# Kernel tuning notes

Measured on AMD Instinct MI355X. Metric: run time of the kernel, lower is better.

The kernel has to match this reference:

```python
import jax, jax.numpy as jnp
import numpy as np

NUM_ROT = 8
OUT_CH = 128
IN_CH = 128
KSIZE = 3


def _resample(filt, angle):
    """Rotate a (O, I, k, k) filter bank by `angle` via bilinear resampling,
    matching F.affine_grid/F.grid_sample with align_corners=True, zero padding."""
    k = filt.shape[-1]
    c, s = jnp.cos(angle), jnp.sin(angle)
    lin = jnp.linspace(-1.0, 1.0, k)
    gy, gx = jnp.meshgrid(lin, lin, indexing='ij')  # (k, k) output coords
    # theta = [[c, -s, 0], [s, c, 0]] applied to (x, y, 1)
    xs = c * gx - s * gy
    ys = s * gx + c * gy
    ix = (xs + 1.0) * 0.5 * (k - 1)  # normalized -> pixel coords
    iy = (ys + 1.0) * 0.5 * (k - 1)
    x0f, y0f = jnp.floor(ix), jnp.floor(iy)
    x0, y0 = x0f.astype(jnp.int32), y0f.astype(jnp.int32)
    wx, wy = ix - x0f, iy - y0f

    def tap(yi, xi, w):
        valid = ((yi >= 0) & (yi < k) & (xi >= 0) & (xi < k)).astype(filt.dtype)
        yc = jnp.clip(yi, 0, k - 1)
        xc = jnp.clip(xi, 0, k - 1)
        return filt[:, :, yc, xc] * (valid * w)  # (O, I, k, k)

    return (tap(y0, x0, (1 - wy) * (1 - wx)) + tap(y0, x0 + 1, (1 - wy) * wx)
            + tap(y0 + 1, x0, wy * (1 - wx)) + tap(y0 + 1, x0 + 1, wy * wx))


def setup_inputs() -> dict:
    key = jax.random.key(0)
    k1, k2, k3 = jax.random.split(key, 3)
    x = jax.random.normal(k1, (16, IN_CH, 128, 128), jnp.float32)
    # base_conv.weight: (out_channels * num_rotations, in_channels, k, k)
    weight = jax.random.normal(k2, (OUT_CH * NUM_ROT, IN_CH, KSIZE, KSIZE), jnp.float32) * 0.05
    rot_alpha = jax.random.normal(k3, (NUM_ROT,), jnp.float32) * 0.1 + 1.0
    return {"x": x, "weight": weight, "rot_alpha": rot_alpha}


def reference(x, weight, rot_alpha):
    R, O, K = NUM_ROT, OUT_CH, KSIZE
    # weight.view(O, R, I, K, K)[:, i] per rotation -> (R, O, I, K, K)
    w_r = weight.reshape(O, R, -1, K, K).transpose(1, 0, 2, 3, 4)
    angles = rot_alpha * (jnp.pi / 4) * jnp.arange(R, dtype=jnp.float32)
    rot_w = jax.vmap(_resample)(w_r, angles)  # (R, O, I, K, K)
    filters = rot_w.reshape(R * O, -1, K, K)
    # one conv with all rotated filter banks instead of R separate convs
    y = jax.lax.conv_general_dilated(
        x, filters, window_strides=(1, 1),
        padding=[(K // 2, K // 2), (K // 2, K // 2)],
        dimension_numbers=('NCHW', 'OIHW', 'NCHW'))  # (B, R*O, H, W)
    B, _, H, W = y.shape
    return y.reshape(B, R, O, H, W).max(axis=1)  # max over rotations
```

## Files before the change

kernel.cpp:

```cpp
#include <hip/hip_runtime.h>

typedef short short8 __attribute__((ext_vector_type(8)));
typedef float f32x4 __attribute__((ext_vector_type(4)));

#define XP_BYTES (16ull * 130 * 130 * 128 * 2)

static __device__ __forceinline__ unsigned short f2bf(float f) {
  unsigned u = __float_as_uint(f);
  u += 0x7FFFu + ((u >> 16) & 1u);
  return (unsigned short)(u >> 16);
}

static __device__ __forceinline__ void gload16(const void* g, void* l) {
  __builtin_amdgcn_global_load_lds(
      (const __attribute__((address_space(1))) void*)g,
      (__attribute__((address_space(3))) void*)l, 16, 0, 0);
}

static __device__ __forceinline__ float wtap(const float* f, int yi, int xi) {
  bool valid = (yi >= 0) & (yi < 3) & (xi >= 0) & (xi < 3);
  int yc = min(max(yi, 0), 2), xc = min(max(xi, 0), 2);
  return valid ? f[yc * 3 + xc] : 0.f;
}

__global__ __launch_bounds__(256) void wprep_kernel(
    const float* __restrict__ w, const float* __restrict__ rot_alpha,
    unsigned short* __restrict__ w2) {
  int gid = blockIdx.x * 256 + threadIdx.x;
  int ic = gid & 127;
  int nr = gid >> 7;
  int r = nr & 7;
  const float* wf = w + (size_t)nr * (128 * 9) + (size_t)ic * 9;
  float f[9];
#pragma unroll
  for (int q = 0; q < 9; ++q) f[q] = wf[q];
  float ang = rot_alpha[r] * 0.78539816339744830962f * (float)r;
  float sth, cth;
  sincosf(ang, &sth, &cth);
#pragma unroll
  for (int j = 0; j < 3; ++j) {
#pragma unroll
    for (int i = 0; i < 3; ++i) {
      float gy = (float)(j - 1), gx = (float)(i - 1);
      float xs = cth * gx - sth * gy;
      float ys = sth * gx + cth * gy;
      float ix = xs + 1.0f, iy = ys + 1.0f;
      float x0f = floorf(ix), y0f = floorf(iy);
      int x0 = (int)x0f, y0 = (int)y0f;
      float wx = ix - x0f, wy = iy - y0f;
      float acc = wtap(f, y0, x0) * (1.f - wy) * (1.f - wx)
                + wtap(f, y0, x0 + 1) * (1.f - wy) * wx
                + wtap(f, y0 + 1, x0) * wy * (1.f - wx)
                + wtap(f, y0 + 1, x0 + 1) * wy * wx;
      w2[(size_t)nr * 1152 + (size_t)(j * 3 + i) * 128 + ic] = f2bf(acc);
    }
  }
}

__global__ __launch_bounds__(256) void xprep_kernel(
    const float* __restrict__ x, unsigned short* __restrict__ xp) {
  const int yy = blockIdx.x;
  const int b = blockIdx.y;
  const int t = threadIdx.x;
  const size_t rowbase = ((size_t)b * 130 + yy) * (130 * 128);
  if (yy == 0 || yy == 129) {
    uint4 z = {0u, 0u, 0u, 0u};
    for (int i = t; i < 2080; i += 256)
      ((uint4*)(xp + rowbase))[i] = z;
    return;
  }
  const int y = yy - 1;
  __shared__ float lt[32][129];
  if (t < 32) {
    uint4 z = {0u, 0u, 0u, 0u};
    int xx = (t < 16) ? 0 : 129;
    int cc = (t & 15) * 8;
    *(uint4*)(xp + rowbase + (size_t)xx * 128 + cc) = z;
  }
  for (int c0 = 0; c0 < 128; c0 += 32) {
#pragma unroll
    for (int i = 0; i < 16; ++i) {
      int idx = i * 256 + t;
      int c = idx >> 7, wq = idx & 127;
      lt[c][wq] = x[(((size_t)b * 128 + c0 + c) * 128 + y) * 128 + wq];
    }
    __syncthreads();
#pragma unroll
    for (int i = 0; i < 2; ++i) {
      int u = i * 256 + t;
      int xx = u >> 2, cp = (u & 3) * 8;
      unsigned short v[8];
#pragma unroll
      for (int q = 0; q < 8; ++q) v[q] = f2bf(lt[cp + q][xx]);
      *(uint4*)(xp + rowbase + (size_t)(xx + 1) * 128 + c0 + cp) = *(uint4*)v;
    }
    __syncthreads();
  }
}

__global__ __launch_bounds__(512, 2) void conv_kernel(
    const unsigned short* __restrict__ xp,
    const unsigned short* __restrict__ w2,
    float* __restrict__ out) {
  __shared__ unsigned short lds[65536];

  const int tid = threadIdx.x;
  const int lane = tid & 63;
  const int wv = tid >> 6;
  const int wr = wv >> 2;
  const int wc = wv & 3;

  const int bid = blockIdx.x;
  const int wg = (bid & 7) * 512 + (bid >> 3);
  const int mblk = wg >> 2;
  const int nblk = wg & 3;
  const int b = mblk >> 6;
  const int y0 = (mblk & 63) << 1;

  const int r0 = tid >> 3;
  const int s0 = tid & 7;
  const int wvoff = wv * 512;

  const unsigned short* xbase = xp + (size_t)(b * 130 + y0) * 130 * 128;
  const unsigned short* wbase = w2 + (size_t)nblk * 256 * 1152;

  const int l15 = lane & 15;
  const int lhi = lane >> 4;
  const int swz = lhi ^ (l15 & 7);

  f32x4 acc[8][4];
#pragma unroll
  for (int mf = 0; mf < 8; ++mf)
#pragma unroll
    for (int nf = 0; nf < 4; ++nf) acc[mf][nf] = (f32x4){0.f, 0.f, 0.f, 0.f};

  auto stage = [&](int pb, int kt) {
    const int tap = kt >> 1;
    const int dy = tap / 3;
    const int dx = tap - dy * 3;
    const int c0 = (kt & 1) << 6;
    unsigned short* la = lds + pb * 16384;
    unsigned short* lb = lds + 32768 + pb * 16384;
#pragma unroll
    for (int hp = 0; hp < 2; ++hp)
#pragma unroll
      for (int i = 0; i < 2; ++i) {
        int r = i * 64 + r0;
        int gs = s0 ^ (r & 7);
        const unsigned short* ga =
            xbase + ((size_t)((hp + dy) * 130) + r + dx) * 128 + c0 + gs * 8;
        gload16(ga, la + hp * 8192 + i * 4096 + wvoff);
      }
#pragma unroll
    for (int hn = 0; hn < 2; ++hn)
#pragma unroll
      for (int i = 0; i < 2; ++i) {
        int r = i * 64 + r0;
        int gs = s0 ^ (r & 7);
        const unsigned short* gb =
            wbase + (size_t)(hn * 128 + r) * 1152 + tap * 128 + c0 + gs * 8;
        gload16(gb, lb + hn * 8192 + i * 4096 + wvoff);
      }
  };

  stage(0, 0);

#pragma unroll 2
  for (int kt = 0; kt < 18; ++kt) {
    const int pb = kt & 1;
    if (kt < 17) {
      stage(pb ^ 1, kt + 1);
      asm volatile("s_waitcnt vmcnt(8)" ::: "memory");
    } else {
      asm volatile("s_waitcnt vmcnt(0)" ::: "memory");
    }
    __builtin_amdgcn_s_barrier();

    const unsigned short* pA = lds + pb * 16384 + wr * 8192 + l15 * 64;
    const unsigned short* pB =
        lds + 32768 + pb * 16384 + (wc >> 1) * 8192 + (wc & 1) * 4096 + l15 * 64;
#pragma unroll
    for (int kk = 0; kk < 2; ++kk) {
      const int sl = (swz ^ (kk << 2)) * 8;
      short8 bf[4];
#pragma unroll
      for (int nf = 0; nf < 4; ++nf)
        bf[nf] = *(const short8*)(pB + nf * 1024 + sl);
#pragma unroll
      for (int mh = 0; mh < 2; ++mh) {
        short8 af[4];
#pragma unroll
        for (int q = 0; q < 4; ++q)
          af[q] = *(const short8*)(pA + (mh * 4 + q) * 1024 + sl);
        __builtin_amdgcn_s_setprio(1);
#pragma unroll
        for (int q = 0; q < 4; ++q)
#pragma unroll
          for (int nf = 0; nf < 4; ++nf)
            acc[mh * 4 + q][nf] = __builtin_amdgcn_mfma_f32_16x16x32_bf16(
                af[q], bf[nf], acc[mh * 4 + q][nf], 0, 0, 0);
        __builtin_amdgcn_s_setprio(0);
      }
    }
    __builtin_amdgcn_s_barrier();
  }

  float* lE = (float*)lds;
#pragma unroll
  for (int mf = 0; mf < 8; ++mf)
#pragma unroll
    for (int nf = 0; nf < 4; ++nf)
#pragma unroll
      for (int j = 0; j < 4; ++j) {
        float v = acc[mf][nf][j];
        v = fmaxf(v, __shfl_xor(v, 1, 64));
        v = fmaxf(v, __shfl_xor(v, 2, 64));
        v = fmaxf(v, __shfl_xor(v, 4, 64));
        if ((lane & 7) == 0) {
          int pix = wr * 128 + mf * 16 + lhi * 4 + j;
          int ol = wc * 8 + nf * 2 + ((lane >> 3) & 1);
          lE[pix * 33 + ol] = v;
        }
      }
  __syncthreads();
  const size_t obase = ((size_t)(b * 128 + nblk * 32) * 128 + y0) * 128;
#pragma unroll
  for (int i = 0; i < 16; ++i) {
    int idx = i * 512 + tid;
    int ol = idx >> 8;
    int pix = idx & 255;
    int yl = pix >> 7;
    int xx = pix & 127;
    out[obase + (size_t)ol * 16384 + yl * 128 + xx] = lE[pix * 33 + ol];
  }
}

extern "C" void kernel_launch(void* const* d_in, const int* in_sizes, int n_in,
                              void* d_out, int out_size, void* d_ws, size_t ws_size,
                              hipStream_t stream) {
  const float* x = (const float*)d_in[0];
  const float* w = (const float*)d_in[1];
  const float* ra = (const float*)d_in[2];
  float* out = (float*)d_out;
  unsigned short* xp = (unsigned short*)d_ws;
  unsigned short* w2 = (unsigned short*)((char*)d_ws + XP_BYTES);

  hipLaunchKernelGGL(wprep_kernel, dim3(512), dim3(256), 0, stream, w, ra, w2);
  hipLaunchKernelGGL(xprep_kernel, dim3(130, 16), dim3(256), 0, stream, x, xp);
  hipLaunchKernelGGL(conv_kernel, dim3(4096), dim3(512), 0, stream, xp, w2, out);
}
```

Baseline: 756.2 us.

## Interleave global-to-LDS loads with MFMA sub-phases using split-K LDS layout

Changes the conv main loop from a whole-tile stage-then-compute schedule to four sub-phases per K-tile. Each sub-phase issues part of the next tile's global-to-LDS loads and runs a 16-MFMA cluster, with barriers and vmcnt waits between them. The LDS layout is reorganized into 32-element k-halves with a new XOR swizzle, and address bases are precomputed. The aim is to hide global-load latency behind MFMA work, at the cost of more barriers per iteration and a finer-grained wait schedule.

```diff
diff --git a/kernel.cpp b/kernel.cpp
--- a/kernel.cpp
+++ b/kernel.cpp
@@ -117,16 +117,22 @@
   const int b = mblk >> 6;
   const int y0 = (mblk & 63) << 1;
 
-  const int r0 = tid >> 3;
-  const int s0 = tid & 7;
+  const int r0 = tid >> 2;
+  const int s0 = tid & 3;
+  const int g0 = s0 ^ ((r0 >> 1) & 3);
   const int wvoff = wv * 512;
 
-  const unsigned short* xbase = xp + (size_t)(b * 130 + y0) * 130 * 128;
-  const unsigned short* wbase = w2 + (size_t)nblk * 256 * 1152;
+  const unsigned short* xpt =
+      xp + (size_t)(b * 130 + y0) * 130 * 128 + r0 * 128 + g0 * 8;
+  const unsigned short* wpt =
+      w2 + (size_t)nblk * 256 * 1152 + (size_t)r0 * 1152 + g0 * 8;
 
   const int l15 = lane & 15;
   const int lhi = lane >> 4;
-  const int swz = lhi ^ (l15 & 7);
+  const int sa = (lhi ^ ((l15 >> 1) & 3)) * 8;
+
+  const int aRd = wr * 8192 + l15 * 32 + sa;
+  const int bRd = 32768 + (wc >> 1) * 8192 + (wc & 1) * 2048 + l15 * 32 + sa;
 
   f32x4 acc[8][4];
 #pragma unroll
@@ -134,76 +140,110 @@
 #pragma unroll
     for (int nf = 0; nf < 4; ++nf) acc[mf][nf] = (f32x4){0.f, 0.f, 0.f, 0.f};
 
-  auto stage = [&](int pb, int kt) {
-    const int tap = kt >> 1;
-    const int dy = tap / 3;
-    const int dx = tap - dy * 3;
-    const int c0 = (kt & 1) << 6;
-    unsigned short* la = lds + pb * 16384;
-    unsigned short* lb = lds + 32768 + pb * 16384;
-#pragma unroll
-    for (int hp = 0; hp < 2; ++hp)
-#pragma unroll
-      for (int i = 0; i < 2; ++i) {
-        int r = i * 64 + r0;
-        int gs = s0 ^ (r & 7);
-        const unsigned short* ga =
-            xbase + ((size_t)((hp + dy) * 130) + r + dx) * 128 + c0 + gs * 8;
-        gload16(ga, la + hp * 8192 + i * 4096 + wvoff);
-      }
-#pragma unroll
-    for (int hn = 0; hn < 2; ++hn)
-#pragma unroll
-      for (int i = 0; i < 2; ++i) {
-        int r = i * 64 + r0;
-        int gs = s0 ^ (r & 7);
-        const unsigned short* gb =
-            wbase + (size_t)(hn * 128 + r) * 1152 + tap * 128 + c0 + gs * 8;
-        gload16(gb, lb + hn * 8192 + i * 4096 + wvoff);
-      }
-  };
-
-  stage(0, 0);
+#define STAGE_A(BUF, HP, KK, DY, DX, CH)                                     \
+  gload16(xpt + ((HP + DY) * 130 + DX) * 128 + (CH) * 64 + (KK) * 32,        \
+          lds + (BUF) * 16384 + (HP) * 8192 + (KK) * 4096 + wvoff)
+#define STAGE_B(BUF, HN, KK, TAP, CH)                                        \
+  gload16(wpt + (size_t)(HN) * 147456 + (TAP) * 128 + (CH) * 64 + (KK) * 32, \
+          lds + 32768 + (BUF) * 16384 + (HN) * 8192 + (KK) * 4096 + wvoff)
+
+  STAGE_A(0, 0, 0, 0, 0, 0);
+  STAGE_A(0, 1, 0, 0, 0, 0);
+  STAGE_B(0, 0, 0, 0, 0);
+  STAGE_B(0, 1, 0, 0, 0);
+  STAGE_A(0, 0, 1, 0, 0, 0);
+  STAGE_A(0, 1, 1, 0, 0, 0);
+  STAGE_B(0, 0, 1, 0, 0);
+  STAGE_B(0, 1, 1, 0, 0);
+  asm volatile("s_waitcnt vmcnt(4)" ::: "memory");
+  __builtin_amdgcn_s_barrier();
 
 #pragma unroll 2
   for (int kt = 0; kt < 18; ++kt) {
-    const int pb = kt & 1;
-    if (kt < 17) {
-      stage(pb ^ 1, kt + 1);
-      asm volatile("s_waitcnt vmcnt(8)" ::: "memory");
-    } else {
-      asm volatile("s_waitcnt vmcnt(0)" ::: "memory");
-    }
-    __builtin_amdgcn_s_barrier();
-
-    const unsigned short* pA = lds + pb * 16384 + wr * 8192 + l15 * 64;
-    const unsigned short* pB =
-        lds + 32768 + pb * 16384 + (wc >> 1) * 8192 + (wc & 1) * 4096 + l15 * 64;
-#pragma unroll
-    for (int kk = 0; kk < 2; ++kk) {
-      const int sl = (swz ^ (kk << 2)) * 8;
-      short8 bf[4];
-#pragma unroll
-      for (int nf = 0; nf < 4; ++nf)
-        bf[nf] = *(const short8*)(pB + nf * 1024 + sl);
-#pragma unroll
-      for (int mh = 0; mh < 2; ++mh) {
-        short8 af[4];
-#pragma unroll
-        for (int q = 0; q < 4; ++q)
-          af[q] = *(const short8*)(pA + (mh * 4 + q) * 1024 + sl);
-        __builtin_amdgcn_s_setprio(1);
-#pragma unroll
-        for (int q = 0; q < 4; ++q)
-#pragma unroll
-          for (int nf = 0; nf < 4; ++nf)
-            acc[mh * 4 + q][nf] = __builtin_amdgcn_mfma_f32_16x16x32_bf16(
-                af[q], bf[nf], acc[mh * 4 + q][nf], 0, 0, 0);
-        __builtin_amdgcn_s_setprio(0);
-      }
-    }
-    __builtin_amdgcn_s_barrier();
-  }
+    const int buf = kt & 1;
+    const bool st = kt < 17;
+    const int nt = kt + 1;
+    const int ntap = nt >> 1;
+    const int nch = nt & 1;
+    const int nbuf = nt & 1;
+    const int ndy = ntap / 3;
+    const int ndx = ntap - ndy * 3;
+
+    const unsigned short* pA = lds + buf * 16384 + aRd;
+    const unsigned short* pB = lds + buf * 16384 + bRd;
+    short8 af[4], bf[4];
+
+#pragma unroll
+    for (int q = 0; q < 4; ++q) af[q] = *(const short8*)(pA + q * 512);
+#pragma unroll
+    for (int nf = 0; nf < 4; ++nf) bf[nf] = *(const short8*)(pB + nf * 512);
+    if (st) { STAGE_A(nbuf, 0, 0, ndy, ndx, nch); STAGE_A(nbuf, 1, 0, ndy, ndx, nch); }
+    __builtin_amdgcn_s_barrier();
+    asm volatile("s_waitcnt lgkmcnt(0)" ::: "memory");
+    __builtin_amdgcn_s_setprio(1);
+#pragma unroll
+    for (int q = 0; q < 4; ++q)
+#pragma unroll
+      for (int nf = 0; nf < 4; ++nf)
+        acc[q][nf] = __builtin_amdgcn_mfma_f32_16x16x32_bf16(af[q], bf[nf],
+                                                             acc[q][nf], 0, 0, 0);
+    __builtin_amdgcn_s_setprio(0);
+    __builtin_amdgcn_s_barrier();
+
+#pragma unroll
+    for (int q = 0; q < 4; ++q) af[q] = *(const short8*)(pA + 2048 + q * 512);
+    if (st) { STAGE_B(nbuf, 0, 0, ntap, nch); STAGE_B(nbuf, 1, 0, ntap, nch); }
+    if (st) asm volatile("s_waitcnt vmcnt(4)" ::: "memory");
+    else    asm volatile("s_waitcnt vmcnt(0)" ::: "memory");
+    __builtin_amdgcn_s_barrier();
+    asm volatile("s_waitcnt lgkmcnt(0)" ::: "memory");
+    __builtin_amdgcn_s_setprio(1);
+#pragma unroll
+    for (int q = 0; q < 4; ++q)
+#pragma unroll
+      for (int nf = 0; nf < 4; ++nf)
+        acc[4 + q][nf] = __builtin_amdgcn_mfma_f32_16x16x32_bf16(
+            af[q], bf[nf], acc[4 + q][nf], 0, 0, 0);
+    __builtin_amdgcn_s_setprio(0);
+    __builtin_amdgcn_s_barrier();
+
+#pragma unroll
+    for (int q = 0; q < 4; ++q) af[q] = *(const short8*)(pA + 4096 + q * 512);
+#pragma unroll
+    for (int nf = 0; nf < 4; ++nf) bf[nf] = *(const short8*)(pB + 4096 + nf * 512);
+    if (st) { STAGE_A(nbuf, 0, 1, ndy, ndx, nch); STAGE_A(nbuf, 1, 1, ndy, ndx, nch); }
+    __builtin_amdgcn_s_barrier();
+    asm volatile("s_waitcnt lgkmcnt(0)" ::: "memory");
+    __builtin_amdgcn_s_setprio(1);
+#pragma unroll
+    for (int q = 0; q < 4; ++q)
+#pragma unroll
+      for (int nf = 0; nf < 4; ++nf)
+        acc[q][nf] = __builtin_amdgcn_mfma_f32_16x16x32_bf16(af[q], bf[nf],
+                                                             acc[q][nf], 0, 0, 0);
+    __builtin_amdgcn_s_setprio(0);
+    __builtin_amdgcn_s_barrier();
+
+#pragma unroll
+    for (int q = 0; q < 4; ++q)
+      af[q] = *(const short8*)(pA + 4096 + 2048 + q * 512);
+    if (st) { STAGE_B(nbuf, 0, 1, ntap, nch); STAGE_B(nbuf, 1, 1, ntap, nch); }
+    if (st) asm volatile("s_waitcnt vmcnt(4)" ::: "memory");
+    else    asm volatile("s_waitcnt vmcnt(0)" ::: "memory");
+    __builtin_amdgcn_s_barrier();
+    asm volatile("s_waitcnt lgkmcnt(0)" ::: "memory");
+    __builtin_amdgcn_s_setprio(1);
+#pragma unroll
+    for (int q = 0; q < 4; ++q)
+#pragma unroll
+      for (int nf = 0; nf < 4; ++nf)
+        acc[4 + q][nf] = __builtin_amdgcn_mfma_f32_16x16x32_bf16(
+            af[q], bf[nf], acc[4 + q][nf], 0, 0, 0);
+    __builtin_amdgcn_s_setprio(0);
+    __builtin_amdgcn_s_barrier();
+  }
+#undef STAGE_A
+#undef STAGE_B
 
   float* lE = (float*)lds;
 #pragma unroll
```

After: 766.5 us. No clear change (+1.4%).
